# Performance work log

Hardware: AMD Instinct MI355X
Metric: run time of the kernel (lower is better)

The kernel has to match this reference:

```python
import jax, jax.numpy as jnp
import numpy as np

B, S, D, H = 2, 512, 1024, 8
DK = D // H
DFF = 4 * D
R = 51
SEP = 64


def setup_inputs() -> dict:
    key = jax.random.key(0)
    ks = jax.random.split(key, 12)
    def w(k, shape, scale=0.02):
        return jax.random.normal(k, shape, jnp.float32) * scale
    return {
        "x": jax.random.normal(ks[0], (B, S, D), jnp.float32),
        "relation": jax.random.randint(ks[1], (B, S, S), 0, R),
        "mask": jnp.ones((B, S, S), jnp.int32),
        "sep_id": SEP,
        "history_reg": jnp.ones((1,), jnp.float32),
        "Wq": w(ks[2], (D, D)), "bq": jnp.zeros((D,), jnp.float32),
        "Wk": w(ks[3], (D, D)), "bk": jnp.zeros((D,), jnp.float32),
        "Wv": w(ks[4], (D, D)), "bv": jnp.zeros((D,), jnp.float32),
        "Wo": w(ks[5], (D, D)), "bo": jnp.zeros((D,), jnp.float32),
        "rel_k_emb": w(ks[6], (R, DK)),
        "rel_v_emb": w(ks[7], (R, DK)),
        "ln1_g": jnp.ones((D,), jnp.float32), "ln1_b": jnp.zeros((D,), jnp.float32),
        "ln2_g": jnp.ones((D,), jnp.float32), "ln2_b": jnp.zeros((D,), jnp.float32),
        "W1": w(ks[8], (D, DFF)), "b1": jnp.zeros((DFF,), jnp.float32),
        "W2": w(ks[9], (DFF, D)), "b2": jnp.zeros((D,), jnp.float32),
    }


def _layer_norm(x, g, b, eps=1e-5):
    m = jnp.mean(x, axis=-1, keepdims=True)
    v = jnp.mean(jnp.square(x - m), axis=-1, keepdims=True)
    return (x - m) * jax.lax.rsqrt(v + eps) * g + b


def _forward(x, relation, mask, sep_id, history_reg, Wq, bq, Wk, bk, Wv, bv, Wo, bo,
             rel_k_emb, rel_v_emb, ln1_g, ln1_b, ln2_g, ln2_b, W1, b1, W2, b2):
    b, s, d = x.shape
    # relation-aware self-attention sublayer (pre-norm)
    h = _layer_norm(x, ln1_g, ln1_b)
    rk = rel_k_emb[relation]  # [B,S,S,DK]
    rv = rel_v_emb[relation]  # [B,S,S,DK]
    def proj(W, bias):
        return (h @ W + bias).reshape(b, s, H, DK).transpose(0, 2, 1, 3)  # [B,H,S,DK]
    q, k, v = proj(Wq, bq), proj(Wk, bk), proj(Wv, bv)
    scores = jnp.einsum("bhid,bhjd->bhij", q, k) + jnp.einsum("bhid,bijd->bhij", q, rk)
    scores = scores / jnp.sqrt(jnp.float32(DK))
    scores = jnp.where(mask[:, None, :, :] == 0, jnp.float32(-1e9), scores)
    attn = jax.nn.softmax(scores, axis=-1)  # [B,H,S,S]
    ctx = jnp.einsum("bhij,bhjd->bhid", attn, v) + jnp.einsum("bhij,bijd->bhid", attn, rv)
    ctx = ctx.transpose(0, 2, 1, 3).reshape(b, s, d)
    attn_out = ctx @ Wo + bo
    # history regularization loss: attention mass on history tokens (positions < sep_id)
    loss = history_reg[0] * jnp.mean(attn[:, :, :, :sep_id])
    x = x + attn_out
    # FFN sublayer (pre-norm)
    h2 = _layer_norm(x, ln2_g, ln2_b)
    ffn = jax.nn.relu(h2 @ W1 + b1) @ W2 + b2
    x = x + ffn
    return x, loss


def reference(x, relation, mask, sep_id, history_reg, Wq, bq, Wk, bk, Wv, bv, Wo, bo,
              rel_k_emb, rel_v_emb, ln1_g, ln1_b, ln2_g, ln2_b, W1, b1, W2, b2):
    return _forward(x, relation, mask, sep_id, history_reg, Wq, bq, Wk, bk, Wv, bv,
                    Wo, bo, rel_k_emb, rel_v_emb, ln1_g, ln1_b, ln2_g, ln2_b,
                    W1, b1, W2, b2)
```

## Files before the change

### kernel.cpp

```cpp
#include <hip/hip_runtime.h>
#include <hip/hip_bf16.h>

#define NB 2
#define NS 512
#define ND 1024
#define NH 8
#define NDK 128
#define NDFF 4096
#define RPAD 64
#define BSROWS 1024
#define NBH 16
#define QT 8
#define SLB 536

typedef __bf16 bf16x8 __attribute__((ext_vector_type(8)));
typedef __bf16 bf16x4 __attribute__((ext_vector_type(4)));
typedef float f32x4 __attribute__((ext_vector_type(4)));

#define BM 64
#define BN 64
#define BK 64

__device__ __forceinline__ void gload16(const void* g, void* l) {
    __builtin_amdgcn_global_load_lds(
        (const __attribute__((address_space(1))) void*)g,
        (__attribute__((address_space(3))) void*)l, 16, 0, 0);
}

__global__ __launch_bounds__(256, 4) void gemm64(
    const __bf16* __restrict__ A, const __bf16* __restrict__ Bt,
    __bf16* __restrict__ vt,
    float* __restrict__ Cf, __bf16* __restrict__ Cb,
    const float* __restrict__ bias,
    int Ksp, int lda, int ldb, int ldc,
    long sA, long sA2, int zdivA,
    long sB, long sB2, int zdivB,
    long sC, int nsplit, long sPart, int flags)
{
    __shared__ __bf16 As0[BM * BK];
    __shared__ __bf16 As1[BM * BK];
    __shared__ __bf16 Bs0[BN * BK];
    __shared__ __bf16 Bs1[BN * BK];

    const unsigned gx = gridDim.x, gy = gridDim.y;
    const unsigned n = gx * gy * gridDim.z;
    const unsigned o = blockIdx.x + gx * (blockIdx.y + gy * blockIdx.z);
    const unsigned q = n >> 3, r = n & 7, xcd = o & 7;
    const unsigned nl = (xcd < r ? xcd * (q + 1) : r * (q + 1) + (xcd - r) * q) + (o >> 3);
    const unsigned bx = nl % gx, tmp = nl / gx;
    const unsigned by = tmp % gy, bz = tmp / gy;

    const int z = bz;
    const int bh = z / nsplit, sp = z - bh * nsplit;
    const long kbase = (long)sp * Ksp;
    A  += (long)(bh / zdivA) * sA + (long)(bh % zdivA) * sA2 + kbase;
    Bt += (long)(bh / zdivB) * sB + (long)(bh % zdivB) * sB2 + kbase;
    const long cbase = (long)bh * sC + (long)sp * sPart;

    const int tM = by * BM, tN = bx * BN;
    const int t = threadIdx.x, lane = t & 63, w = t >> 6;
    const int wr = w >> 1, wc = w & 1;

    const int srow = lane >> 3;
    const int scolE = ((((lane & 7) << 4) ^ (srow << 4)) >> 1);

    const __bf16* gA = A + (long)(tM + srow) * lda + scolE;
    const __bf16* gB = Bt + (long)(tN + srow) * ldb + scolE;

    f32x4 acc[2][2];
#pragma unroll
    for (int m = 0; m < 2; ++m)
#pragma unroll
        for (int nn = 0; nn < 2; ++nn)
#pragma unroll
            for (int j = 0; j < 4; ++j) acc[m][nn][j] = 0.f;

    const int r16 = lane & 15;
    const int kq = (lane >> 4) * 8;
    const int xorE = (r16 & 7) * 8;
    const int nt = Ksp / BK;

    auto STAGE = [&](__bf16* as, __bf16* bs, int k0) {
#pragma unroll
        for (int i = 0; i < 2; ++i) {
            const int rr = (w + i * 4) * 8;
            gload16(gA + (long)rr * lda + k0, (void*)&as[rr * BK]);
            gload16(gB + (long)rr * ldb + k0, (void*)&bs[rr * BK]);
        }
    };
    auto COMPUTE = [&](const __bf16* as, const __bf16* bs) {
        __builtin_amdgcn_s_setprio(1);
#pragma unroll
        for (int ks = 0; ks < 2; ++ks) {
            bf16x8 af[2], bv[2];
#pragma unroll
            for (int m = 0; m < 2; ++m)
                af[m] = *(const bf16x8*)&as[(wr * 32 + m * 16 + r16) * BK + ((ks * 32 + kq) ^ xorE)];
#pragma unroll
            for (int nn = 0; nn < 2; ++nn)
                bv[nn] = *(const bf16x8*)&bs[(wc * 32 + nn * 16 + r16) * BK + ((ks * 32 + kq) ^ xorE)];
#pragma unroll
            for (int m = 0; m < 2; ++m)
#pragma unroll
                for (int nn = 0; nn < 2; ++nn)
                    acc[m][nn] = __builtin_amdgcn_mfma_f32_16x16x32_bf16(af[m], bv[nn], acc[m][nn], 0, 0, 0);
        }
        __builtin_amdgcn_s_setprio(0);
    };

    STAGE(As0, Bs0, 0);
    STAGE(As1, Bs1, BK);
    for (int tt = 0; tt < nt; tt += 2) {
        asm volatile("s_waitcnt vmcnt(4)\n\ts_barrier" ::: "memory");
        COMPUTE(As0, Bs0);
        asm volatile("s_waitcnt lgkmcnt(0)\n\ts_barrier" ::: "memory");
        const bool more = (tt + 2 < nt);
        if (more) {
            STAGE(As0, Bs0, (tt + 2) * BK);
            asm volatile("s_waitcnt vmcnt(4)\n\ts_barrier" ::: "memory");
        } else {
            asm volatile("s_waitcnt vmcnt(0)\n\ts_barrier" ::: "memory");
        }
        COMPUTE(As1, Bs1);
        asm volatile("s_waitcnt lgkmcnt(0)\n\ts_barrier" ::: "memory");
        if (more) STAGE(As1, Bs1, (tt + 3) * BK);
    }

    const bool relu = (flags & 1) != 0;
    const bool vmode = (flags & 8) && (tN >= 2 * ND);
#pragma unroll
    for (int m = 0; m < 2; ++m) {
        const int gr0 = tM + wr * 32 + m * 16 + (lane >> 4) * 4;
#pragma unroll
        for (int nn = 0; nn < 2; ++nn) {
            const int gc = tN + wc * 32 + nn * 16 + (lane & 15);
            const float bb = bias ? bias[gc] : 0.f;
            if (vmode) {
                const int hd = gc - 2 * ND;
                const int b = gr0 >> 9, i = gr0 & 511;
                bf16x4 ov;
#pragma unroll
                for (int j = 0; j < 4; ++j) ov[j] = (__bf16)(acc[m][nn][j] + bb);
                *(bf16x4*)&vt[(((long)b * NH + (hd >> 7)) * NDK + (hd & 127)) * NS + i] = ov;
            } else {
#pragma unroll
                for (int j = 0; j < 4; ++j) {
                    float v = acc[m][nn][j] + bb;
                    if (relu) v = fmaxf(v, 0.f);
                    const long idx = cbase + (long)(gr0 + j) * ldc + gc;
                    if (Cb) Cb[idx] = (__bf16)v;
                    else Cf[idx] = v;
                }
            }
        }
    }
}

__global__ __launch_bounds__(256, 4) void attn_fused(
    const __bf16* __restrict__ qkvb, const __bf16* __restrict__ vt,
    const __bf16* __restrict__ relkT, const __bf16* __restrict__ relvT,
    const int* __restrict__ relation, const int* __restrict__ mask,
    __bf16* __restrict__ ctxm, float* __restrict__ loss_part,
    const int* __restrict__ sep_p)
{
    __shared__ __bf16 Sl[QT * SLB];
    __shared__ float qrl[QT][RPAD];
    __shared__ float bins[QT][68];
    __shared__ float redl[4];

    const unsigned o = blockIdx.x + 64u * blockIdx.y;
    const unsigned nl = (o & 7) * 128u + (o >> 3);
    const int qt = nl & 63, bh = nl >> 6;
    const int b = bh >> 3, h = bh & 7;
    const int i0 = qt * QT;

    const int t = threadIdx.x, lane = t & 63, w = t >> 6;
    const int r16 = lane & 15;
    const int r8 = r16 & 7;
    const int kq = (lane >> 4) * 8;
    const int sep = *sep_p;

    bf16x8 qf[4];
    {
        const __bf16* qrow = qkvb + ((long)(b * NS + i0 + r8)) * (3 * ND) + h * NDK;
#pragma unroll
        for (int ks = 0; ks < 4; ++ks)
            qf[ks] = *(const bf16x8*)(qrow + ks * 32 + kq);
    }

    int4 ra[2][2], ma[2][2];
#pragma unroll
    for (int rr = 0; rr < 2; ++rr) {
        const long rg = (long)(b * NS + i0 + w * 2 + rr) * NS;
        ra[rr][0] = ((const int4*)(relation + rg))[lane * 2];
        ra[rr][1] = ((const int4*)(relation + rg))[lane * 2 + 1];
        ma[rr][0] = ((const int4*)(mask + rg))[lane * 2];
        ma[rr][1] = ((const int4*)(mask + rg))[lane * 2 + 1];
    }

    const int brow = t & 7;
    const int bj0 = (t >> 3) * 16;
    int4 br[4];
    {
        const int4* rp = (const int4*)(relation + ((long)(b * NS + i0 + brow)) * NS + bj0);
#pragma unroll
        for (int c = 0; c < 4; ++c) br[c] = rp[c];
    }

    {
        f32x4 a;
#pragma unroll
        for (int j = 0; j < 4; ++j) a[j] = 0.f;
#pragma unroll
        for (int ks = 0; ks < 4; ++ks) {
            const bf16x8 bfr = *(const bf16x8*)(relkT + (long)(w * 16 + r16) * NDK + ks * 32 + kq);
            a = __builtin_amdgcn_mfma_f32_16x16x32_bf16(qf[ks], bfr, a, 0, 0, 0);
        }
#pragma unroll
        for (int j = 0; j < 4; ++j) {
            const int row = (lane >> 4) * 4 + j;
            if (row < QT) qrl[row][w * 16 + (lane & 15)] = a[j];
        }
    }
    for (int idx = t; idx < QT * 68; idx += 256) ((float*)bins)[idx] = 0.f;

    {
        const __bf16* kb = qkvb + ((long)(b * NS + w * 16 + r16)) * (3 * ND) + ND + h * NDK;
#pragma unroll
        for (int tt = 0; tt < 8; ++tt) {
            const __bf16* krow = kb + (long)(tt * 64) * (3 * ND);
            f32x4 s;
#pragma unroll
            for (int j = 0; j < 4; ++j) s[j] = 0.f;
#pragma unroll
            for (int ks = 0; ks < 4; ++ks) {
                const bf16x8 bfr = *(const bf16x8*)(krow + ks * 32 + kq);
                s = __builtin_amdgcn_mfma_f32_16x16x32_bf16(qf[ks], bfr, s, 0, 0, 0);
            }
            const int colb = tt * 64 + w * 16 + (lane & 15);
#pragma unroll
            for (int j = 0; j < 4; ++j) {
                const int row = (lane >> 4) * 4 + j;
                if (row < QT) Sl[row * SLB + colb] = (__bf16)s[j];
            }
        }
    }
    __syncthreads();

    const float sc = 0.088388347648318447f;
    float lsum = 0.f;
#pragma unroll
    for (int rr = 0; rr < 2; ++rr) {
        const int row = w * 2 + rr;
        const bf16x8 sv = *(const bf16x8*)&Sl[row * SLB + lane * 8];
        int rl[8], mm[8];
        rl[0] = ra[rr][0].x; rl[1] = ra[rr][0].y; rl[2] = ra[rr][0].z; rl[3] = ra[rr][0].w;
        rl[4] = ra[rr][1].x; rl[5] = ra[rr][1].y; rl[6] = ra[rr][1].z; rl[7] = ra[rr][1].w;
        mm[0] = ma[rr][0].x; mm[1] = ma[rr][0].y; mm[2] = ma[rr][0].z; mm[3] = ma[rr][0].w;
        mm[4] = ma[rr][1].x; mm[5] = ma[rr][1].y; mm[6] = ma[rr][1].z; mm[7] = ma[rr][1].w;
        float v[8];
        float mx = -1e30f;
#pragma unroll
        for (int q = 0; q < 8; ++q) {
            float vv = ((float)sv[q] + qrl[row][rl[q]]) * sc;
            if (mm[q] == 0) vv = -1e9f;
            v[q] = vv;
            mx = fmaxf(mx, vv);
        }
#pragma unroll
        for (int of = 32; of > 0; of >>= 1) mx = fmaxf(mx, __shfl_xor(mx, of, 64));
        float sm = 0.f;
#pragma unroll
        for (int q = 0; q < 8; ++q) { v[q] = __expf(v[q] - mx); sm += v[q]; }
#pragma unroll
        for (int of = 32; of > 0; of >>= 1) sm += __shfl_xor(sm, of, 64);
        const float inv = 1.f / sm;
        bf16x8 av;
#pragma unroll
        for (int q = 0; q < 8; ++q) {
            const float a = v[q] * inv;
            av[q] = (__bf16)a;
            if (lane * 8 + q < sep) lsum += a;
        }
        *(bf16x8*)&Sl[row * SLB + lane * 8] = av;
    }
#pragma unroll
    for (int of = 32; of > 0; of >>= 1) lsum += __shfl_xor(lsum, of, 64);
    if (lane == 0) redl[w] = lsum;
    __syncthreads();
    if (t == 0) loss_part[bh * 64 + qt] = redl[0] + redl[1] + redl[2] + redl[3];

    {
        const __bf16* ap = &Sl[brow * SLB + bj0];
#pragma unroll
        for (int c = 0; c < 4; ++c) {
            const bf16x4 a4 = *(const bf16x4*)(ap + c * 4);
            atomicAdd(&bins[brow][br[c].x], (float)a4[0]);
            atomicAdd(&bins[brow][br[c].y], (float)a4[1]);
            atomicAdd(&bins[brow][br[c].z], (float)a4[2]);
            atomicAdd(&bins[brow][br[c].w], (float)a4[3]);
        }
    }

    f32x4 oacc[2];
#pragma unroll
    for (int nn = 0; nn < 2; ++nn)
#pragma unroll
        for (int j = 0; j < 4; ++j) oacc[nn][j] = 0.f;

    {
        const __bf16* vb = vt + ((long)bh * NDK + w * 32 + r16) * NS;
#pragma unroll
        for (int tt = 0; tt < 8; ++tt) {
#pragma unroll
            for (int ks = 0; ks < 2; ++ks) {
                const bf16x8 af = *(const bf16x8*)&Sl[r8 * SLB + tt * 64 + ks * 32 + kq];
#pragma unroll
                for (int nn = 0; nn < 2; ++nn) {
                    const bf16x8 bv = *(const bf16x8*)(vb + (long)(nn * 16) * NS + tt * 64 + ks * 32 + kq);
                    oacc[nn] = __builtin_amdgcn_mfma_f32_16x16x32_bf16(af, bv, oacc[nn], 0, 0, 0);
                }
            }
        }
    }
    __syncthreads();

#pragma unroll
    for (int kc = 0; kc < 2; ++kc) {
        const float4 b0 = *(const float4*)&bins[r8][kc * 32 + kq];
        const float4 b1 = *(const float4*)&bins[r8][kc * 32 + kq + 4];
        bf16x8 af;
        af[0] = (__bf16)b0.x; af[1] = (__bf16)b0.y; af[2] = (__bf16)b0.z; af[3] = (__bf16)b0.w;
        af[4] = (__bf16)b1.x; af[5] = (__bf16)b1.y; af[6] = (__bf16)b1.z; af[7] = (__bf16)b1.w;
#pragma unroll
        for (int nn = 0; nn < 2; ++nn) {
            const bf16x8 bfr = *(const bf16x8*)(relvT + (long)(w * 32 + nn * 16 + r16) * RPAD + kc * 32 + kq);
            oacc[nn] = __builtin_amdgcn_mfma_f32_16x16x32_bf16(af, bfr, oacc[nn], 0, 0, 0);
        }
    }
#pragma unroll
    for (int nn = 0; nn < 2; ++nn)
#pragma unroll
        for (int j = 0; j < 4; ++j) {
            const int row = (lane >> 4) * 4 + j;
            if (row < QT)
                ctxm[((long)(b * NS + i0 + row)) * ND + h * NDK + w * 32 + nn * 16 + (lane & 15)] =
                    (__bf16)oacc[nn][j];
        }
}

__global__ void prep_weights(
    const float* __restrict__ Wq, const float* __restrict__ Wk,
    const float* __restrict__ Wv, const float* __restrict__ Wo,
    const float* __restrict__ W1, const float* __restrict__ W2,
    const float* __restrict__ relv,
    const float* __restrict__ bq, const float* __restrict__ bk,
    const float* __restrict__ bv, const float* __restrict__ relk,
    const float* __restrict__ x, const float* __restrict__ ln1g,
    const float* __restrict__ ln1b,
    __bf16* __restrict__ WqkvT, __bf16* __restrict__ WoT,
    __bf16* __restrict__ W1T, __bf16* __restrict__ W2T,
    __bf16* __restrict__ relvT, float* __restrict__ biasqkv,
    __bf16* __restrict__ relkT, __bf16* __restrict__ h1, int R)
{
    const int tile = blockIdx.x;
    const int t = threadIdx.y * 32 + threadIdx.x;

    if (tile >= 12372) {
        const long row = tile - 12372;
        const float* xr = x + row * ND;
        float4 v = reinterpret_cast<const float4*>(xr)[t];
        float s = v.x + v.y + v.z + v.w;
        float s2 = v.x * v.x + v.y * v.y + v.z * v.z + v.w * v.w;
#pragma unroll
        for (int o = 32; o > 0; o >>= 1) {
            s += __shfl_xor(s, o, 64);
            s2 += __shfl_xor(s2, o, 64);
        }
        __shared__ float red[8];
        const int lane = t & 63, wv = t >> 6;
        if (lane == 0) { red[wv] = s; red[4 + wv] = s2; }
        __syncthreads();
        s = red[0] + red[1] + red[2] + red[3];
        s2 = red[4] + red[5] + red[6] + red[7];
        const float mean = s * (1.f / ND);
        const float var = s2 * (1.f / ND) - mean * mean;
        const float rs = rsqrtf(var + 1e-5f);
        const float xv[4] = {v.x, v.y, v.z, v.w};
        bf16x4 o;
#pragma unroll
        for (int j = 0; j < 4; ++j) {
            const int c = t * 4 + j;
            o[j] = (__bf16)((xv[j] - mean) * rs * ln1g[c] + ln1b[c]);
        }
        *(bf16x4*)&h1[row * ND + t * 4] = o;
        return;
    }
    if (tile >= 12296) {
        const int ft = (tile - 12296) * 256 + t;
        if (ft < ND) biasqkv[ft] = bq[ft];
        else if (ft < 2 * ND) biasqkv[ft] = bk[ft - ND];
        else if (ft < 3 * ND) biasqkv[ft] = bv[ft - 2 * ND];
        else {
            const int idx = ft - 3 * ND;
            if (idx < 128 * NDK) {
                const int r = idx / NDK;
                relkT[idx] = (r < R) ? (__bf16)relk[idx] : (__bf16)0.f;
            }
        }
        return;
    }
    const float* src; __bf16* dst;
    int rows_in, cols_in, ldo, kx, ny;
    if (tile < 4096) {
        const int m = tile >> 10, r = tile & 1023;
        kx = r & 31; ny = r >> 5;
        rows_in = 1024; cols_in = 1024; ldo = 1024;
        src = m == 0 ? Wq : m == 1 ? Wk : m == 2 ? Wv : Wo;
        dst = m == 3 ? WoT : WqkvT + (size_t)m * 1024 * 1024;
    } else if (tile < 8192) {
        const int r = tile - 4096;
        kx = r & 31; ny = r >> 5;
        rows_in = 1024; cols_in = 4096; ldo = 1024; src = W1; dst = W1T;
    } else if (tile < 12288) {
        const int r = tile - 8192;
        kx = r & 127; ny = r >> 7;
        rows_in = 4096; cols_in = 1024; ldo = 4096; src = W2; dst = W2T;
    } else {
        const int r = tile - 12288;
        kx = r & 1; ny = r >> 1;
        rows_in = R; cols_in = 128; ldo = 64; src = relv; dst = relvT;
    }

    __shared__ float tl[32][33];
    const int k0 = kx * 32, n0 = ny * 32;
    const int tx = threadIdx.x, ty = threadIdx.y;
#pragma unroll
    for (int dy = 0; dy < 32; dy += 8) {
        const int k = k0 + ty + dy, nn = n0 + tx;
        tl[ty + dy][tx] = (k < rows_in && nn < cols_in) ? src[(long)k * cols_in + nn] : 0.f;
    }
    __syncthreads();
#pragma unroll
    for (int dy = 0; dy < 32; dy += 8) {
        const int nn = n0 + ty + dy, k = k0 + tx;
        if (nn < cols_in && k < ldo) dst[(long)nn * ldo + k] = (__bf16)tl[tx][ty + dy];
    }
}

__global__ __launch_bounds__(256) void wo_reduce_ln(
    const float* __restrict__ P, const float* __restrict__ x,
    const float* __restrict__ bo, const float* __restrict__ g,
    const float* __restrict__ bb, float* __restrict__ out,
    __bf16* __restrict__ h2)
{
    const int row = blockIdx.x;
    const int t = threadIdx.x;
    const long i4 = (long)row * 256 + t;
    const long sP = (long)BSROWS * ND / 4;
    const float4* P4 = (const float4*)P;
    float4 s = P4[i4];
    const float4 t1 = P4[i4 + sP];
    s.x += t1.x; s.y += t1.y; s.z += t1.z; s.w += t1.w;
    const int col = t * 4;
    const float4 xv = ((const float4*)x)[i4];
    const float4 bv = *(const float4*)&bo[col];
    float4 o;
    o.x = s.x + xv.x + bv.x; o.y = s.y + xv.y + bv.y;
    o.z = s.z + xv.z + bv.z; o.w = s.w + xv.w + bv.w;
    ((float4*)out)[i4] = o;

    float sum = o.x + o.y + o.z + o.w;
    float sum2 = o.x * o.x + o.y * o.y + o.z * o.z + o.w * o.w;
#pragma unroll
    for (int of = 32; of > 0; of >>= 1) {
        sum += __shfl_xor(sum, of, 64);
        sum2 += __shfl_xor(sum2, of, 64);
    }
    __shared__ float red[8];
    const int lane = t & 63, wv = t >> 6;
    if (lane == 0) { red[wv] = sum; red[4 + wv] = sum2; }
    __syncthreads();
    sum = red[0] + red[1] + red[2] + red[3];
    sum2 = red[4] + red[5] + red[6] + red[7];
    const float mean = sum * (1.f / ND);
    const float var = sum2 * (1.f / ND) - mean * mean;
    const float rs = rsqrtf(var + 1e-5f);
    const float ov[4] = {o.x, o.y, o.z, o.w};
    bf16x4 hb;
#pragma unroll
    for (int j = 0; j < 4; ++j)
        hb[j] = (__bf16)((ov[j] - mean) * rs * g[col + j] + bb[col + j]);
    *(bf16x4*)&h2[(long)row * ND + col] = hb;
}

__global__ __launch_bounds__(256) void ffn2_reduce(
    const float* __restrict__ P, const float* __restrict__ b2, float* __restrict__ out,
    const float* __restrict__ loss_part, const float* __restrict__ hist,
    const int* __restrict__ sep_p, float* __restrict__ out_loss)
{
    const int i4 = blockIdx.x * 256 + threadIdx.x;
    const long sP = (long)BSROWS * ND / 4;
    const float4* P4 = (const float4*)P;
    float4 s = P4[i4];
    const float4 t1 = P4[i4 + sP];
    s.x += t1.x; s.y += t1.y; s.z += t1.z; s.w += t1.w;
    const int col = (i4 * 4) & (ND - 1);
    const float4 bv = *(const float4*)&b2[col];
    float4 o = ((float4*)out)[i4];
    o.x += s.x + bv.x; o.y += s.y + bv.y;
    o.z += s.z + bv.z; o.w += s.w + bv.w;
    ((float4*)out)[i4] = o;

    if (blockIdx.x == 0) {
        const int t = threadIdx.x;
        const float4 v = ((const float4*)loss_part)[t];
        float ls = v.x + v.y + v.z + v.w;
#pragma unroll
        for (int of = 32; of > 0; of >>= 1) ls += __shfl_xor(ls, of, 64);
        __shared__ float red[4];
        if ((t & 63) == 0) red[t >> 6] = ls;
        __syncthreads();
        if (t == 0) {
            const int sep = *sep_p;
            const float total = red[0] + red[1] + red[2] + red[3];
            const float denom = (float)NB * NH * NS * (float)(sep > 0 ? sep : 1);
            out_loss[0] = (sep > 0) ? hist[0] * total / denom : 0.f;
        }
    }
}

extern "C" void kernel_launch(void* const* d_in, const int* in_sizes, int n_in,
                              void* d_out, int out_size, void* d_ws, size_t ws_size,
                              hipStream_t stream)
{
    const float* x      = (const float*)d_in[0];
    const int* relation = (const int*)d_in[1];
    const int* mask     = (const int*)d_in[2];
    const int* sep_p    = (const int*)d_in[3];
    const float* hist   = (const float*)d_in[4];
    const float* Wq = (const float*)d_in[5],  *bq = (const float*)d_in[6];
    const float* Wk = (const float*)d_in[7],  *bk = (const float*)d_in[8];
    const float* Wv = (const float*)d_in[9],  *bv = (const float*)d_in[10];
    const float* Wo = (const float*)d_in[11], *bo = (const float*)d_in[12];
    const float* relk = (const float*)d_in[13];
    const float* relv = (const float*)d_in[14];
    const float* ln1g = (const float*)d_in[15], *ln1b = (const float*)d_in[16];
    const float* ln2g = (const float*)d_in[17], *ln2b = (const float*)d_in[18];
    const float* W1 = (const float*)d_in[19], *b1 = (const float*)d_in[20];
    const float* W2 = (const float*)d_in[21], *b2 = (const float*)d_in[22];
    const int R = in_sizes[13] / NDK;

    float* out = (float*)d_out;
    float* out_loss = out + (long)BSROWS * ND;

    char* p = (char*)d_ws;
    auto alloc = [&](size_t bytes) -> void* {
        void* r = (void*)p;
        p += (bytes + 255) & ~(size_t)255;
        return r;
    };
    __bf16* WqkvT   = (__bf16*)alloc((size_t)3 * ND * ND * 2);
    __bf16* WoT     = (__bf16*)alloc((size_t)ND * ND * 2);
    __bf16* W1T     = (__bf16*)alloc((size_t)NDFF * ND * 2);
    __bf16* W2T     = (__bf16*)alloc((size_t)ND * NDFF * 2);
    __bf16* relkT   = (__bf16*)alloc((size_t)128 * NDK * 2);
    __bf16* relvT   = (__bf16*)alloc((size_t)NDK * RPAD * 2);
    float*  biasqkv = (float*)alloc((size_t)3 * ND * 4);
    __bf16* h1      = (__bf16*)alloc((size_t)BSROWS * ND * 2);
    __bf16* qkvb    = (__bf16*)alloc((size_t)BSROWS * 3 * ND * 2);
    __bf16* vt      = (__bf16*)alloc((size_t)NBH * NDK * NS * 2);
    __bf16* ctxm    = (__bf16*)alloc((size_t)BSROWS * ND * 2);
    __bf16* h2      = (__bf16*)alloc((size_t)BSROWS * ND * 2);
    __bf16* F1      = (__bf16*)alloc((size_t)BSROWS * NDFF * 2);
    float*  loss_part = (float*)alloc((size_t)1024 * 4);
    float*  arena   = (float*)alloc((size_t)16 * 1024 * 1024);
    float* woPart   = arena;
    float* f2Part   = arena + (size_t)2 * 1024 * 1024;

    const dim3 tb(32, 8);
    prep_weights<<<13396, tb, 0, stream>>>(Wq, Wk, Wv, Wo, W1, W2, relv,
                                           bq, bk, bv, relk, x, ln1g, ln1b,
                                           WqkvT, WoT, W1T, W2T, relvT,
                                           biasqkv, relkT, h1, R);

    gemm64<<<dim3(48, 16, 1), 256, 0, stream>>>(
        h1, WqkvT, vt, nullptr, qkvb, biasqkv,
        ND, ND, ND, 3 * ND,
        0, 0, 1, 0, 0, 1, 0, 1, 0, 8);

    attn_fused<<<dim3(64, 16), 256, 0, stream>>>(
        qkvb, vt, relkT, relvT, relation, mask, ctxm, loss_part, sep_p);

    gemm64<<<dim3(16, 16, 2), 256, 0, stream>>>(
        ctxm, WoT, nullptr, woPart, nullptr, nullptr,
        512, ND, ND, ND,
        0, 0, 1, 0, 0, 1,
        0, 2, (long)BSROWS * ND, 0);

    wo_reduce_ln<<<BSROWS, 256, 0, stream>>>(woPart, x, bo, ln2g, ln2b, out, h2);

    gemm64<<<dim3(64, 16, 1), 256, 0, stream>>>(
        h2, W1T, nullptr, nullptr, F1, b1,
        ND, ND, ND, NDFF,
        0, 0, 1, 0, 0, 1, 0, 1, 0, 1);

    gemm64<<<dim3(16, 16, 2), 256, 0, stream>>>(
        F1, W2T, nullptr, f2Part, nullptr, nullptr,
        2048, NDFF, NDFF, ND,
        0, 0, 1, 0, 0, 1,
        0, 2, (long)BSROWS * ND, 0);

    ffn2_reduce<<<1024, 256, 0, stream>>>(f2Part, b2, out,
                                          loss_part, hist, sep_p, out_loss);
}
```

Baseline: 140.0 us.

## Split attention over key/value chunks with flash-decoding style combine kernel

Replaces the single fused attention kernel with a split-KV version that processes 128-key chunks per block (4x more blocks) and writes partial outputs, relation bins, max, sum and loss partials to global memory. A new combine kernel rescales the partials with log-sum-exp weights, applies the relation-value projection in scalar FP32, and writes the context. The goal is more parallelism and higher occupancy (launch bounds raised to 8 waves per EU). The cost is an extra launch and extra global traffic for the FP32 partials.

```diff
diff --git a/kernel.cpp b/kernel.cpp
--- a/kernel.cpp
+++ b/kernel.cpp
@@ -11,7 +11,7 @@
 #define BSROWS 1024
 #define NBH 16
 #define QT 8
-#define SLB 536
+#define KVS 128
 
 typedef __bf16 bf16x8 __attribute__((ext_vector_type(8)));
 typedef __bf16 bf16x4 __attribute__((ext_vector_type(4)));
@@ -156,27 +156,30 @@
     }
 }
 
-__global__ __launch_bounds__(256, 4) void attn_fused(
+__global__ __launch_bounds__(256, 8) void attn_split(
     const __bf16* __restrict__ qkvb, const __bf16* __restrict__ vt,
-    const __bf16* __restrict__ relkT, const __bf16* __restrict__ relvT,
+    const __bf16* __restrict__ relkT,
     const int* __restrict__ relation, const int* __restrict__ mask,
-    __bf16* __restrict__ ctxm, float* __restrict__ loss_part,
-    const int* __restrict__ sep_p)
+    float* __restrict__ oPart, float* __restrict__ binsPart,
+    float* __restrict__ mPart, float* __restrict__ sPart,
+    float* __restrict__ lPart, const int* __restrict__ sep_p)
 {
-    __shared__ __bf16 Sl[QT * SLB];
+    __shared__ __bf16 Sl[QT][136];
     __shared__ float qrl[QT][RPAD];
     __shared__ float bins[QT][68];
-    __shared__ float redl[4];
-
-    const unsigned o = blockIdx.x + 64u * blockIdx.y;
-    const unsigned nl = (o & 7) * 128u + (o >> 3);
-    const int qt = nl & 63, bh = nl >> 6;
+
+    const unsigned o = blockIdx.x + 64u * (blockIdx.y + 4u * blockIdx.z);
+    const unsigned nl = (o & 7) * 512u + (o >> 3);
+    const int qt = nl & 63;
+    const int sp = (nl >> 6) & 3;
+    const int bh = nl >> 8;
     const int b = bh >> 3, h = bh & 7;
     const int i0 = qt * QT;
+    const int kv0 = sp * KVS;
+    const long pblk = (long)(bh * 64 + qt) * 4 + sp;
 
     const int t = threadIdx.x, lane = t & 63, w = t >> 6;
-    const int r16 = lane & 15;
-    const int r8 = r16 & 7;
+    const int r16 = lane & 15, r8 = r16 & 7;
     const int kq = (lane >> 4) * 8;
     const int sep = *sep_p;
 
@@ -188,25 +191,6 @@
             qf[ks] = *(const bf16x8*)(qrow + ks * 32 + kq);
     }
 
-    int4 ra[2][2], ma[2][2];
-#pragma unroll
-    for (int rr = 0; rr < 2; ++rr) {
-        const long rg = (long)(b * NS + i0 + w * 2 + rr) * NS;
-        ra[rr][0] = ((const int4*)(relation + rg))[lane * 2];
-        ra[rr][1] = ((const int4*)(relation + rg))[lane * 2 + 1];
-        ma[rr][0] = ((const int4*)(mask + rg))[lane * 2];
-        ma[rr][1] = ((const int4*)(mask + rg))[lane * 2 + 1];
-    }
-
-    const int brow = t & 7;
-    const int bj0 = (t >> 3) * 16;
-    int4 br[4];
-    {
-        const int4* rp = (const int4*)(relation + ((long)(b * NS + i0 + brow)) * NS + bj0);
-#pragma unroll
-        for (int c = 0; c < 4; ++c) br[c] = rp[c];
-    }
-
     {
         f32x4 a;
 #pragma unroll
@@ -224,82 +208,70 @@
     }
     for (int idx = t; idx < QT * 68; idx += 256) ((float*)bins)[idx] = 0.f;
 
-    {
-        const __bf16* kb = qkvb + ((long)(b * NS + w * 16 + r16)) * (3 * ND) + ND + h * NDK;
-#pragma unroll
-        for (int tt = 0; tt < 8; ++tt) {
-            const __bf16* krow = kb + (long)(tt * 64) * (3 * ND);
-            f32x4 s;
-#pragma unroll
-            for (int j = 0; j < 4; ++j) s[j] = 0.f;
-#pragma unroll
-            for (int ks = 0; ks < 4; ++ks) {
-                const bf16x8 bfr = *(const bf16x8*)(krow + ks * 32 + kq);
-                s = __builtin_amdgcn_mfma_f32_16x16x32_bf16(qf[ks], bfr, s, 0, 0, 0);
-            }
-            const int colb = tt * 64 + w * 16 + (lane & 15);
-#pragma unroll
-            for (int j = 0; j < 4; ++j) {
-                const int row = (lane >> 4) * 4 + j;
-                if (row < QT) Sl[row * SLB + colb] = (__bf16)s[j];
-            }
+#pragma unroll
+    for (int tt = 0; tt < 2; ++tt) {
+        const int col = kv0 + tt * 64 + w * 16 + r16;
+        const __bf16* krow = qkvb + ((long)(b * NS + col)) * (3 * ND) + ND + h * NDK;
+        f32x4 s;
+#pragma unroll
+        for (int j = 0; j < 4; ++j) s[j] = 0.f;
+#pragma unroll
+        for (int ks = 0; ks < 4; ++ks) {
+            const bf16x8 bfr = *(const bf16x8*)(krow + ks * 32 + kq);
+            s = __builtin_amdgcn_mfma_f32_16x16x32_bf16(qf[ks], bfr, s, 0, 0, 0);
+        }
+        const int colL = tt * 64 + w * 16 + (lane & 15);
+#pragma unroll
+        for (int j = 0; j < 4; ++j) {
+            const int row = (lane >> 4) * 4 + j;
+            if (row < QT) Sl[row][colL] = (__bf16)s[j];
         }
     }
     __syncthreads();
 
     const float sc = 0.088388347648318447f;
-    float lsum = 0.f;
 #pragma unroll
     for (int rr = 0; rr < 2; ++rr) {
         const int row = w * 2 + rr;
-        const bf16x8 sv = *(const bf16x8*)&Sl[row * SLB + lane * 8];
-        int rl[8], mm[8];
-        rl[0] = ra[rr][0].x; rl[1] = ra[rr][0].y; rl[2] = ra[rr][0].z; rl[3] = ra[rr][0].w;
-        rl[4] = ra[rr][1].x; rl[5] = ra[rr][1].y; rl[6] = ra[rr][1].z; rl[7] = ra[rr][1].w;
-        mm[0] = ma[rr][0].x; mm[1] = ma[rr][0].y; mm[2] = ma[rr][0].z; mm[3] = ma[rr][0].w;
-        mm[4] = ma[rr][1].x; mm[5] = ma[rr][1].y; mm[6] = ma[rr][1].z; mm[7] = ma[rr][1].w;
-        float v[8];
-        float mx = -1e30f;
-#pragma unroll
-        for (int q = 0; q < 8; ++q) {
-            float vv = ((float)sv[q] + qrl[row][rl[q]]) * sc;
-            if (mm[q] == 0) vv = -1e9f;
-            v[q] = vv;
-            mx = fmaxf(mx, vv);
-        }
+        const long rg = (long)(b * NS + i0 + row) * NS + kv0;
+        const int2 rl2 = *(const int2*)(relation + rg + lane * 2);
+        const int2 mm2 = *(const int2*)(mask + rg + lane * 2);
+        float v0 = ((float)Sl[row][lane * 2] + qrl[row][rl2.x]) * sc;
+        float v1 = ((float)Sl[row][lane * 2 + 1] + qrl[row][rl2.y]) * sc;
+        if (mm2.x == 0) v0 = -1e9f;
+        if (mm2.y == 0) v1 = -1e9f;
+        float mx = fmaxf(v0, v1);
 #pragma unroll
         for (int of = 32; of > 0; of >>= 1) mx = fmaxf(mx, __shfl_xor(mx, of, 64));
-        float sm = 0.f;
-#pragma unroll
-        for (int q = 0; q < 8; ++q) { v[q] = __expf(v[q] - mx); sm += v[q]; }
-#pragma unroll
-        for (int of = 32; of > 0; of >>= 1) sm += __shfl_xor(sm, of, 64);
-        const float inv = 1.f / sm;
-        bf16x8 av;
-#pragma unroll
-        for (int q = 0; q < 8; ++q) {
-            const float a = v[q] * inv;
-            av[q] = (__bf16)a;
-            if (lane * 8 + q < sep) lsum += a;
-        }
-        *(bf16x8*)&Sl[row * SLB + lane * 8] = av;
-    }
-#pragma unroll
-    for (int of = 32; of > 0; of >>= 1) lsum += __shfl_xor(lsum, of, 64);
-    if (lane == 0) redl[w] = lsum;
+        const float e0 = __expf(v0 - mx), e1 = __expf(v1 - mx);
+        float sm = e0 + e1;
+        float ls = 0.f;
+        if (kv0 + lane * 2 < sep) ls += e0;
+        if (kv0 + lane * 2 + 1 < sep) ls += e1;
+#pragma unroll
+        for (int of = 32; of > 0; of >>= 1) {
+            sm += __shfl_xor(sm, of, 64);
+            ls += __shfl_xor(ls, of, 64);
+        }
+        Sl[row][lane * 2] = (__bf16)e0;
+        Sl[row][lane * 2 + 1] = (__bf16)e1;
+        if (lane == 0) {
+            mPart[pblk * QT + row] = mx;
+            sPart[pblk * QT + row] = sm;
+            lPart[pblk * QT + row] = ls;
+        }
+    }
     __syncthreads();
-    if (t == 0) loss_part[bh * 64 + qt] = redl[0] + redl[1] + redl[2] + redl[3];
 
     {
-        const __bf16* ap = &Sl[brow * SLB + bj0];
-#pragma unroll
-        for (int c = 0; c < 4; ++c) {
-            const bf16x4 a4 = *(const bf16x4*)(ap + c * 4);
-            atomicAdd(&bins[brow][br[c].x], (float)a4[0]);
-            atomicAdd(&bins[brow][br[c].y], (float)a4[1]);
-            atomicAdd(&bins[brow][br[c].z], (float)a4[2]);
-            atomicAdd(&bins[brow][br[c].w], (float)a4[3]);
-        }
+        const int brow = t & 7;
+        const int bj0 = (t >> 3) * 4;
+        const int4 br = *(const int4*)(relation + ((long)(b * NS + i0 + brow)) * NS + kv0 + bj0);
+        const bf16x4 a4 = *(const bf16x4*)&Sl[brow][bj0];
+        atomicAdd(&bins[brow][br.x], (float)a4[0]);
+        atomicAdd(&bins[brow][br.y], (float)a4[1]);
+        atomicAdd(&bins[brow][br.z], (float)a4[2]);
+        atomicAdd(&bins[brow][br.w], (float)a4[3]);
     }
 
     f32x4 oacc[2];
@@ -307,46 +279,118 @@
     for (int nn = 0; nn < 2; ++nn)
 #pragma unroll
         for (int j = 0; j < 4; ++j) oacc[nn][j] = 0.f;
-
     {
-        const __bf16* vb = vt + ((long)bh * NDK + w * 32 + r16) * NS;
-#pragma unroll
-        for (int tt = 0; tt < 8; ++tt) {
-#pragma unroll
-            for (int ks = 0; ks < 2; ++ks) {
-                const bf16x8 af = *(const bf16x8*)&Sl[r8 * SLB + tt * 64 + ks * 32 + kq];
-#pragma unroll
-                for (int nn = 0; nn < 2; ++nn) {
-                    const bf16x8 bv = *(const bf16x8*)(vb + (long)(nn * 16) * NS + tt * 64 + ks * 32 + kq);
-                    oacc[nn] = __builtin_amdgcn_mfma_f32_16x16x32_bf16(af, bv, oacc[nn], 0, 0, 0);
-                }
+        const __bf16* vb = vt + ((long)bh * NDK + w * 32 + r16) * NS + kv0;
+#pragma unroll
+        for (int ks = 0; ks < 4; ++ks) {
+            const bf16x8 af = *(const bf16x8*)&Sl[r8][ks * 32 + kq];
+#pragma unroll
+            for (int nn = 0; nn < 2; ++nn) {
+                const bf16x8 bv = *(const bf16x8*)(vb + (long)(nn * 16) * NS + ks * 32 + kq);
+                oacc[nn] = __builtin_amdgcn_mfma_f32_16x16x32_bf16(af, bv, oacc[nn], 0, 0, 0);
             }
         }
     }
     __syncthreads();
 
-#pragma unroll
-    for (int kc = 0; kc < 2; ++kc) {
-        const float4 b0 = *(const float4*)&bins[r8][kc * 32 + kq];
-        const float4 b1 = *(const float4*)&bins[r8][kc * 32 + kq + 4];
-        bf16x8 af;
-        af[0] = (__bf16)b0.x; af[1] = (__bf16)b0.y; af[2] = (__bf16)b0.z; af[3] = (__bf16)b0.w;
-        af[4] = (__bf16)b1.x; af[5] = (__bf16)b1.y; af[6] = (__bf16)b1.z; af[7] = (__bf16)b1.w;
-#pragma unroll
-        for (int nn = 0; nn < 2; ++nn) {
-            const bf16x8 bfr = *(const bf16x8*)(relvT + (long)(w * 32 + nn * 16 + r16) * RPAD + kc * 32 + kq);
-            oacc[nn] = __builtin_amdgcn_mfma_f32_16x16x32_bf16(af, bfr, oacc[nn], 0, 0, 0);
-        }
-    }
 #pragma unroll
     for (int nn = 0; nn < 2; ++nn)
 #pragma unroll
         for (int j = 0; j < 4; ++j) {
             const int row = (lane >> 4) * 4 + j;
             if (row < QT)
-                ctxm[((long)(b * NS + i0 + row)) * ND + h * NDK + w * 32 + nn * 16 + (lane & 15)] =
-                    (__bf16)oacc[nn][j];
-        }
+                oPart[pblk * (QT * KVS) + row * KVS + w * 32 + nn * 16 + (lane & 15)] = oacc[nn][j];
+        }
+    for (int idx = t; idx < QT * 64; idx += 256)
+        binsPart[pblk * (QT * 64) + idx] = bins[idx >> 6][idx & 63];
+}
+
+__global__ __launch_bounds__(256) void attn_combine(
+    const float* __restrict__ oPart, const float* __restrict__ binsPart,
+    const float* __restrict__ mPart, const float* __restrict__ sPart,
+    const float* __restrict__ lPart, const __bf16* __restrict__ relvT,
+    __bf16* __restrict__ ctxm, float* __restrict__ loss_part)
+{
+    __shared__ float cf[4][QT];
+    __shared__ float binsF[QT][68];
+    __shared__ float lrow[QT];
+
+    const int cb = blockIdx.x;
+    const int bh = cb >> 6, qt = cb & 63;
+    const int b = bh >> 3, h = bh & 7;
+    const int i0 = qt * QT;
+    const int t = threadIdx.x;
+    const long pb = (long)cb * 4;
+
+    if (t < QT) {
+        float m[4], s[4], l[4];
+#pragma unroll
+        for (int sp = 0; sp < 4; ++sp) {
+            m[sp] = mPart[(pb + sp) * QT + t];
+            s[sp] = sPart[(pb + sp) * QT + t];
+            l[sp] = lPart[(pb + sp) * QT + t];
+        }
+        const float M = fmaxf(fmaxf(m[0], m[1]), fmaxf(m[2], m[3]));
+        float Z = 0.f;
+#pragma unroll
+        for (int sp = 0; sp < 4; ++sp) Z += s[sp] * __expf(m[sp] - M);
+        const float invZ = 1.f / Z;
+        float lo = 0.f;
+#pragma unroll
+        for (int sp = 0; sp < 4; ++sp) {
+            const float c = __expf(m[sp] - M) * invZ;
+            cf[sp][t] = c;
+            lo += l[sp] * c;
+        }
+        lrow[t] = lo;
+    }
+    __syncthreads();
+    if (t == 0) {
+        float s = 0.f;
+#pragma unroll
+        for (int r = 0; r < QT; ++r) s += lrow[r];
+        loss_part[cb] = s;
+    }
+
+    for (int idx = t; idx < QT * 64; idx += 256) {
+        const int row = idx >> 6;
+        float v = 0.f;
+#pragma unroll
+        for (int sp = 0; sp < 4; ++sp)
+            v += binsPart[(pb + sp) * (QT * 64) + idx] * cf[sp][row];
+        binsF[row][idx & 63] = v;
+    }
+
+    const int row = t >> 5;
+    const int c4 = (t & 31) * 4;
+    float4 oo = {0.f, 0.f, 0.f, 0.f};
+#pragma unroll
+    for (int sp = 0; sp < 4; ++sp) {
+        const float4 op = *(const float4*)&oPart[(pb + sp) * (QT * KVS) + row * KVS + c4];
+        const float c = cf[sp][row];
+        oo.x += op.x * c; oo.y += op.y * c; oo.z += op.z * c; oo.w += op.w * c;
+    }
+    __syncthreads();
+
+    float dt[4];
+#pragma unroll
+    for (int k = 0; k < 4; ++k) {
+        const __bf16* rv = relvT + (long)(c4 + k) * RPAD;
+        float acc = 0.f;
+#pragma unroll
+        for (int q = 0; q < 8; ++q) {
+            const bf16x8 r8v = *(const bf16x8*)(rv + q * 8);
+#pragma unroll
+            for (int e = 0; e < 8; ++e) acc += binsF[row][q * 8 + e] * (float)r8v[e];
+        }
+        dt[k] = acc;
+    }
+    bf16x4 outv;
+    outv[0] = (__bf16)(oo.x + dt[0]);
+    outv[1] = (__bf16)(oo.y + dt[1]);
+    outv[2] = (__bf16)(oo.z + dt[2]);
+    outv[3] = (__bf16)(oo.w + dt[3]);
+    *(bf16x4*)&ctxm[((long)(b * NS + i0 + row)) * ND + h * NDK + c4] = outv;
 }
 
 __global__ void prep_weights(
@@ -574,9 +618,13 @@
     __bf16* h2      = (__bf16*)alloc((size_t)BSROWS * ND * 2);
     __bf16* F1      = (__bf16*)alloc((size_t)BSROWS * NDFF * 2);
     float*  loss_part = (float*)alloc((size_t)1024 * 4);
-    float*  arena   = (float*)alloc((size_t)16 * 1024 * 1024);
-    float* woPart   = arena;
-    float* f2Part   = arena + (size_t)2 * 1024 * 1024;
+    float*  oPart   = (float*)alloc((size_t)4096 * QT * KVS * 4);
+    float*  binsPart= (float*)alloc((size_t)4096 * QT * 64 * 4);
+    float*  mPart   = (float*)alloc((size_t)4096 * QT * 4);
+    float*  sPart   = (float*)alloc((size_t)4096 * QT * 4);
+    float*  lPart   = (float*)alloc((size_t)4096 * QT * 4);
+    float*  woPart  = (float*)alloc((size_t)2 * BSROWS * ND * 4);
+    float*  f2Part  = (float*)alloc((size_t)2 * BSROWS * ND * 4);
 
     const dim3 tb(32, 8);
     prep_weights<<<13396, tb, 0, stream>>>(Wq, Wk, Wv, Wo, W1, W2, relv,
@@ -589,8 +637,12 @@
         ND, ND, ND, 3 * ND,
         0, 0, 1, 0, 0, 1, 0, 1, 0, 8);
 
-    attn_fused<<<dim3(64, 16), 256, 0, stream>>>(
-        qkvb, vt, relkT, relvT, relation, mask, ctxm, loss_part, sep_p);
+    attn_split<<<dim3(64, 4, 16), 256, 0, stream>>>(
+        qkvb, vt, relkT, relation, mask,
+        oPart, binsPart, mPart, sPart, lPart, sep_p);
+
+    attn_combine<<<1024, 256, 0, stream>>>(
+        oPart, binsPart, mPart, sPart, lPart, relvT, ctxm, loss_part);
 
     gemm64<<<dim3(16, 16, 2), 256, 0, stream>>>(
         ctxm, WoT, nullptr, woPart, nullptr, nullptr,
```

After: 164.2 us. 17.3% more time.
